# Kernel optimization log

Measured on AMD Instinct MI355X. Metric: run time of the kernel, lower is better.

The kernel has to match this reference:

```python
import jax, jax.numpy as jnp
import numpy as np

GN_EPS = 1e-5
G = 8          # SKA groups
SKS3 = 27      # sks**3


def _aff(x, s, b):
    # folded BatchNorm (eval): per-channel scale + shift on NCDHW tensor
    return x * s[None, :, None, None, None] + b[None, :, None, None, None]


def _c1(x, w):
    # 1x1x1 conv as channel GEMM; w: [O, I]
    return jnp.einsum('bcdhw,oc->bodhw', x, w)


def _dw5(x, w):
    # depthwise 5x5x5 conv, pad=2; w: [C, 1, 5, 5, 5]
    return jax.lax.conv_general_dilated(
        x, w, window_strides=(1, 1, 1), padding=[(2, 2)] * 3,
        dimension_numbers=('NCDHW', 'OIDHW', 'NCDHW'),
        feature_group_count=x.shape[1])


def setup_inputs() -> dict:
    key = jax.random.key(0)
    ks = jax.random.split(key, 24)
    B, C, D, H, W = 2, 64, 32, 32, 32

    def n(k, shape, scale=1.0):
        return jax.random.normal(k, shape, jnp.float32) * scale

    def u(k, shape):
        return jax.random.uniform(k, shape, jnp.float32, 0.5, 1.5)

    return {
        'x': n(ks[0], (B, C, D, H, W)),
        'w1': n(ks[1], (32, 64), 64 ** -0.5),
        's1': u(ks[2], (32,)), 'b1': n(ks[3], (32,), 0.1),
        'w2': n(ks[4], (32, 1, 5, 5, 5), 125 ** -0.5),
        's2': u(ks[5], (32,)), 'b2': n(ks[6], (32,), 0.1),
        'w3': n(ks[7], (32, 32), 32 ** -0.5),
        's3': u(ks[8], (32,)), 'b3': n(ks[9], (32,), 0.1),
        'w4': n(ks[10], (216, 32), 32 ** -0.5), 'b4': n(ks[11], (216,), 0.1),
        'gn_g': u(ks[12], (216,)), 'gn_b': n(ks[13], (216,), 0.1),
        'bn_s': u(ks[14], (64,)), 'bn_b': n(ks[15], (64,), 0.1),
        'pw1_w': n(ks[16], (128, 64), 64 ** -0.5),
        'pw1_s': u(ks[17], (128,)), 'pw1_b': n(ks[18], (128,), 0.1),
        'pw2_w': n(ks[19], (64, 128), 128 ** -0.5),
        'pw2_s': u(ks[20], (64,)), 'pw2_b': n(ks[21], (64,), 0.1),
    }


def reference(x, w1, s1, b1, w2, s2, b2, w3, s3, b3, w4, b4,
              gn_g, gn_b, bn_s, bn_b,
              pw1_w, pw1_s, pw1_b, pw2_w, pw2_s, pw2_b):
    B, C, D, H, W = x.shape

    # ---- LKP3D: dynamic kernel generation ----
    a = jax.nn.relu(_aff(_c1(x, w1), s1, b1))          # cv1 + BN + ReLU
    a = _aff(_dw5(a, w2), s2, b2)                      # cv2 (5^3 dw) + BN
    a = jax.nn.relu(_aff(_c1(a, w3), s3, b3))          # cv3 + BN + ReLU
    wk = _c1(a, w4) + b4[None, :, None, None, None]    # cv4: [B,216,D,H,W]
    # GroupNorm: num_groups = dim//groups = 8, channels = 216
    g = wk.reshape(B, G, SKS3, D, H, W)
    mu = g.mean(axis=(2, 3, 4, 5), keepdims=True)
    var = g.var(axis=(2, 3, 4, 5), keepdims=True)
    g = (g - mu) * jax.lax.rsqrt(var + GN_EPS)
    wk = g.reshape(B, G * SKS3, D, H, W) * gn_g[None, :, None, None, None] \
         + gn_b[None, :, None, None, None]
    wk = wk.reshape(B, G, SKS3, D, H, W)               # [B, G, 27, D, H, W]

    # ---- SKA3D: apply dynamic kernels (27 shifted copies, grouped) ----
    offs = [(di, hi, wi) for di in (-1, 0, 1) for hi in (-1, 0, 1) for wi in (-1, 0, 1)]
    patches = jnp.stack(
        [jnp.roll(x, (-di, -hi, -wi), axis=(2, 3, 4)) for di, hi, wi in offs],
        axis=2)                                        # [B, C, 27, D, H, W]
    p = patches.reshape(B, G, C // G, SKS3, D, H, W)
    sk = jnp.einsum('bgckdhw,bgkdhw->bgcdhw', p, wk).reshape(B, C, D, H, W)

    y = _aff(sk, bn_s, bn_b) + x                       # LSConv BN + residual

    # ---- FFN (residual): pw1 + BN + ReLU + pw2 + BN ----
    f = jax.nn.relu(_aff(_c1(y, pw1_w), pw1_s, pw1_b))
    f = _aff(_c1(f, pw2_w), pw2_s, pw2_b)
    return y + f
```

## Files before the change

### kernel.cpp

```cpp
#include <hip/hip_runtime.h>

#define SPAT 32768
#define BATCH 2
#define GN_EPS 1e-5f

__device__ __forceinline__ void fma4(float4& a, const float4& v, float w) {
    a.x = fmaf(v.x, w, a.x); a.y = fmaf(v.y, w, a.y);
    a.z = fmaf(v.z, w, a.z); a.w = fmaf(v.w, w, a.w);
}

__global__ __launch_bounds__(64) void k_zero(float* __restrict__ p)
{
    if (threadIdx.x < 32) p[threadIdx.x] = 0.f;
}

template <int CIN, int NO, bool RELU>
__global__ __launch_bounds__(256) void k_c1(
    const float* __restrict__ in, const float* __restrict__ w,
    const float* __restrict__ sc, const float* __restrict__ bi,
    float* __restrict__ out, int Cout)
{
    int q = blockIdx.x * 256 + threadIdx.x;
    int s = q * 4;
    int o0 = blockIdx.y * NO, b = blockIdx.z;
    const float* ip = in + (size_t)b * CIN * SPAT + s;
    float4 acc[NO];
#pragma unroll
    for (int i = 0; i < NO; ++i) acc[i] = {0.f, 0.f, 0.f, 0.f};
#pragma unroll 4
    for (int c = 0; c < CIN; ++c) {
        float4 v = *(const float4*)(ip + (size_t)c * SPAT);
#pragma unroll
        for (int i = 0; i < NO; ++i)
            fma4(acc[i], v, w[(o0 + i) * CIN + c]);
    }
#pragma unroll
    for (int i = 0; i < NO; ++i) {
        int o = o0 + i;
        float scale = sc[o], shift = bi[o];
        float4 r = acc[i];
        r.x = r.x * scale + shift; r.y = r.y * scale + shift;
        r.z = r.z * scale + shift; r.w = r.w * scale + shift;
        if (RELU) {
            r.x = fmaxf(r.x, 0.f); r.y = fmaxf(r.y, 0.f);
            r.z = fmaxf(r.z, 0.f); r.w = fmaxf(r.w, 0.f);
        }
        *(float4*)(out + ((size_t)b * Cout + o) * SPAT + s) = r;
    }
}

__global__ __launch_bounds__(256) void k_cv4_stats(
    const float* __restrict__ a, const float* __restrict__ w4,
    const float* __restrict__ b4, float* __restrict__ stats)
{
    int q = blockIdx.x * 256 + threadIdx.x;
    int s = q * 4;
    int g = blockIdx.y, b = blockIdx.z;
    const float* ip = a + (size_t)b * 32 * SPAT + s;
    const float* wg = w4 + g * 27 * 32;
    float4 wk[27];
#pragma unroll
    for (int k = 0; k < 27; ++k) {
        float bv = b4[g * 27 + k];
        wk[k] = {bv, bv, bv, bv};
    }
#pragma unroll 2
    for (int c = 0; c < 32; ++c) {
        float4 v = *(const float4*)(ip + (size_t)c * SPAT);
#pragma unroll
        for (int k = 0; k < 27; ++k)
            fma4(wk[k], v, wg[k * 32 + c]);
    }
    float sum = 0.f, ss = 0.f;
#pragma unroll
    for (int k = 0; k < 27; ++k) {
        sum += wk[k].x + wk[k].y + wk[k].z + wk[k].w;
        ss  += wk[k].x * wk[k].x + wk[k].y * wk[k].y
             + wk[k].z * wk[k].z + wk[k].w * wk[k].w;
    }
#pragma unroll
    for (int off = 32; off > 0; off >>= 1) {
        sum += __shfl_down(sum, off, 64);
        ss  += __shfl_down(ss,  off, 64);
    }
    __shared__ float sh[8];
    int wave = threadIdx.x >> 6, lane = threadIdx.x & 63;
    if (lane == 0) { sh[wave * 2] = sum; sh[wave * 2 + 1] = ss; }
    __syncthreads();
    if (threadIdx.x == 0) {
        int bg = b * 8 + g;
        atomicAdd(&stats[bg * 2 + 0], sh[0] + sh[2] + sh[4] + sh[6]);
        atomicAdd(&stats[bg * 2 + 1], sh[1] + sh[3] + sh[5] + sh[7]);
    }
}

__global__ __launch_bounds__(256) void k_ska(
    const float* __restrict__ x, const float* __restrict__ a1,
    const float* __restrict__ w4, const float* __restrict__ b4,
    const float* __restrict__ stats,
    const float* __restrict__ gn_g, const float* __restrict__ gn_b,
    const float* __restrict__ bn_s, const float* __restrict__ bn_b,
    float* __restrict__ y)
{
    int q = blockIdx.x * 256 + threadIdx.x;
    int s = q * 4;
    int g = blockIdx.y, b = blockIdx.z;
    int bg = b * 8 + g;
    const float N = 27.f * (float)SPAT;
    float mu  = stats[bg * 2 + 0] / N;
    float var = stats[bg * 2 + 1] / N - mu * mu;
    float inv = rsqrtf(var + GN_EPS);
    int d = s >> 10, h = (s >> 5) & 31, w0 = s & 31;
    int lane = threadIdx.x & 63;
    int xl_src = (lane & 56) | ((lane + 7) & 7);
    int xr_src = (lane & 56) | ((lane + 1) & 7);
    const float* xg = x + ((size_t)(b * 64 + g * 8)) * SPAT;
    const float* ag = a1 + (size_t)b * 32 * SPAT + s;
    const float* wg = w4 + g * 27 * 32;

    float4 acc[8];
    float4 xc[8];
#pragma unroll
    for (int c = 0; c < 8; ++c) acc[c] = {0.f, 0.f, 0.f, 0.f};

#pragma unroll
    for (int kd = 0; kd < 3; ++kd) {
        float4 wk9[9];
#pragma unroll
        for (int j = 0; j < 9; ++j) {
            float bv = b4[g * 27 + kd * 9 + j];
            wk9[j] = {bv, bv, bv, bv};
        }
#pragma unroll 4
        for (int c = 0; c < 32; ++c) {
            float4 v = *(const float4*)(ag + (size_t)c * SPAT);
#pragma unroll
            for (int j = 0; j < 9; ++j)
                fma4(wk9[j], v, wg[(kd * 9 + j) * 32 + c]);
        }
#pragma unroll
        for (int j = 0; j < 9; ++j) {
            int kk = kd * 9 + j;
            float gg = gn_g[g * 27 + kk] * inv;
            float sgb = gn_b[g * 27 + kk] - mu * gg;
            wk9[j].x = wk9[j].x * gg + sgb;
            wk9[j].y = wk9[j].y * gg + sgb;
            wk9[j].z = wk9[j].z * gg + sgb;
            wk9[j].w = wk9[j].w * gg + sgb;
        }
        int zd = (d + kd + 31) & 31;
#pragma unroll
        for (int kh = 0; kh < 3; ++kh) {
            int zh = (h + kh + 31) & 31;
            int rowoff = zd * 1024 + zh * 32;
            bool center = (kd == 1) && (kh == 1);
#pragma unroll
            for (int c = 0; c < 8; ++c) {
                float4 m = *(const float4*)(xg + (size_t)c * SPAT + rowoff + w0);
                if (center) xc[c] = m;
                float xl = __shfl(m.w, xl_src, 64);
                float xr = __shfl(m.x, xr_src, 64);
                float win[6] = {xl, m.x, m.y, m.z, m.w, xr};
#pragma unroll
                for (int kw = 0; kw < 3; ++kw) {
                    float4 wn = wk9[kh * 3 + kw];
                    acc[c].x = fmaf(win[0 + kw], wn.x, acc[c].x);
                    acc[c].y = fmaf(win[1 + kw], wn.y, acc[c].y);
                    acc[c].z = fmaf(win[2 + kw], wn.z, acc[c].z);
                    acc[c].w = fmaf(win[3 + kw], wn.w, acc[c].w);
                }
            }
        }
    }
#pragma unroll
    for (int c = 0; c < 8; ++c) {
        int ch = g * 8 + c;
        float bs = bn_s[ch], bb = bn_b[ch];
        float4 r;
        r.x = acc[c].x * bs + bb + xc[c].x;
        r.y = acc[c].y * bs + bb + xc[c].y;
        r.z = acc[c].z * bs + bb + xc[c].z;
        r.w = acc[c].w * bs + bb + xc[c].w;
        *(float4*)(y + ((size_t)(b * 64 + ch)) * SPAT + s) = r;
    }
}

__global__ __launch_bounds__(256) void k_dw5(
    const float* __restrict__ in, const float* __restrict__ w2,
    const float* __restrict__ s2, const float* __restrict__ b2,
    float* __restrict__ out)
{
    __shared__ float lds[8 * 36 * 40];
    int tid = threadIdx.x;
    int d0 = blockIdx.x * 4;
    int c = blockIdx.y, b = blockIdx.z;
    const float* ip = in + ((size_t)(b * 32 + c)) * SPAT;

    float4 z = {0.f, 0.f, 0.f, 0.f};
    for (int i = tid; i < 8 * 36 * 40 / 4; i += 256)
        ((float4*)lds)[i] = z;
    __syncthreads();
    for (int i = tid; i < 8 * 256; i += 256) {
        int p = i >> 8, rem = i & 255;
        int r = rem >> 3, c4 = (rem & 7) * 4;
        int d = d0 - 2 + p;
        if (d >= 0 && d < 32) {
            float4 v = *(const float4*)(ip + d * 1024 + r * 32 + c4);
            *(float4*)&lds[p * 1440 + (r + 2) * 40 + (c4 + 4)] = v;
        }
    }
    __syncthreads();

    float scl = s2[c], shf = b2[c];
    const float* wt = w2 + c * 125;
#pragma unroll
    for (int k = 0; k < 4; ++k) {
        int j = tid + k * 256;
        int pd = j >> 8, rem = j & 255;
        int hr = rem >> 3, w4i = (rem & 7) * 4;
        float4 acc = {0.f, 0.f, 0.f, 0.f};
#pragma unroll
        for (int kd = 0; kd < 5; ++kd) {
            const float* pl = &lds[(pd + kd) * 1440];
#pragma unroll
            for (int kh = 0; kh < 5; ++kh) {
                const float* row = pl + (hr + kh) * 40 + w4i;
                float4 r0 = *(const float4*)(row);
                float4 r1 = *(const float4*)(row + 4);
                float4 r2 = *(const float4*)(row + 8);
                float win[12] = {r0.x, r0.y, r0.z, r0.w,
                                 r1.x, r1.y, r1.z, r1.w,
                                 r2.x, r2.y, r2.z, r2.w};
#pragma unroll
                for (int kw = 0; kw < 5; ++kw) {
                    float wv = wt[kd * 25 + kh * 5 + kw];
                    acc.x = fmaf(wv, win[2 + 0 + kw], acc.x);
                    acc.y = fmaf(wv, win[2 + 1 + kw], acc.y);
                    acc.z = fmaf(wv, win[2 + 2 + kw], acc.z);
                    acc.w = fmaf(wv, win[2 + 3 + kw], acc.w);
                }
            }
        }
        acc.x = acc.x * scl + shf; acc.y = acc.y * scl + shf;
        acc.z = acc.z * scl + shf; acc.w = acc.w * scl + shf;
        *(float4*)(out + ((size_t)(b * 32 + c)) * SPAT
                   + (d0 + pd) * 1024 + hr * 32 + w4i) = acc;
    }
}

template <int NO>
__global__ __launch_bounds__(256) void k_pw2_out(
    const float* __restrict__ f1, const float* __restrict__ w,
    const float* __restrict__ sc, const float* __restrict__ bi,
    const float* __restrict__ yres, float* __restrict__ out)
{
    int q = blockIdx.x * 256 + threadIdx.x;
    int s = q * 4;
    int o0 = blockIdx.y * NO, b = blockIdx.z;
    const float* ip = f1 + (size_t)b * 128 * SPAT + s;
    float4 acc[NO];
#pragma unroll
    for (int i = 0; i < NO; ++i) acc[i] = {0.f, 0.f, 0.f, 0.f};
#pragma unroll 4
    for (int c = 0; c < 128; ++c) {
        float4 v = *(const float4*)(ip + (size_t)c * SPAT);
#pragma unroll
        for (int i = 0; i < NO; ++i)
            fma4(acc[i], v, w[(o0 + i) * 128 + c]);
    }
#pragma unroll
    for (int i = 0; i < NO; ++i) {
        int o = o0 + i;
        float scale = sc[o], shift = bi[o];
        float4 yv = *(const float4*)(yres + ((size_t)(b * 64 + o)) * SPAT + s);
        float4 r = acc[i];
        r.x = r.x * scale + shift + yv.x;
        r.y = r.y * scale + shift + yv.y;
        r.z = r.z * scale + shift + yv.z;
        r.w = r.w * scale + shift + yv.w;
        *(float4*)(out + ((size_t)(b * 64 + o)) * SPAT + s) = r;
    }
}

extern "C" void kernel_launch(void* const* d_in, const int* in_sizes, int n_in,
                              void* d_out, int out_size, void* d_ws, size_t ws_size,
                              hipStream_t stream)
{
    const float* x     = (const float*)d_in[0];
    const float* w1    = (const float*)d_in[1];
    const float* s1    = (const float*)d_in[2];
    const float* b1    = (const float*)d_in[3];
    const float* w2    = (const float*)d_in[4];
    const float* s2    = (const float*)d_in[5];
    const float* b2    = (const float*)d_in[6];
    const float* w3    = (const float*)d_in[7];
    const float* s3    = (const float*)d_in[8];
    const float* b3    = (const float*)d_in[9];
    const float* w4    = (const float*)d_in[10];
    const float* b4    = (const float*)d_in[11];
    const float* gn_g  = (const float*)d_in[12];
    const float* gn_b  = (const float*)d_in[13];
    const float* bn_s  = (const float*)d_in[14];
    const float* bn_b  = (const float*)d_in[15];
    const float* pw1_w = (const float*)d_in[16];
    const float* pw1_s = (const float*)d_in[17];
    const float* pw1_b = (const float*)d_in[18];
    const float* pw2_w = (const float*)d_in[19];
    const float* pw2_s = (const float*)d_in[20];
    const float* pw2_b = (const float*)d_in[21];

    float* ws    = (float*)d_ws;
    float* a1    = ws;
    float* a2    = a1 + (size_t)BATCH * 32 * SPAT;
    float* yb    = a2 + (size_t)BATCH * 32 * SPAT;
    float* f1    = yb + (size_t)BATCH * 64 * SPAT;
    float* stats = f1 + (size_t)BATCH * 128 * SPAT;

    dim3 blk(256);
    k_zero<<<dim3(1), dim3(64), 0, stream>>>(stats);
    k_c1<64, 8, true><<<dim3(SPAT / 1024, 4, BATCH), blk, 0, stream>>>(
        x, w1, s1, b1, a1, 32);
    k_dw5<<<dim3(8, 32, BATCH), blk, 0, stream>>>(a1, w2, s2, b2, a2);
    k_c1<32, 8, true><<<dim3(SPAT / 1024, 4, BATCH), blk, 0, stream>>>(
        a2, w3, s3, b3, a1, 32);
    k_cv4_stats<<<dim3(SPAT / 1024, 8, BATCH), blk, 0, stream>>>(
        a1, w4, b4, stats);
    k_ska<<<dim3(SPAT / 1024, 8, BATCH), blk, 0, stream>>>(
        x, a1, w4, b4, stats, gn_g, gn_b, bn_s, bn_b, yb);
    k_c1<64, 16, true><<<dim3(SPAT / 1024, 8, BATCH), blk, 0, stream>>>(
        yb, pw1_w, pw1_s, pw1_b, f1, 128);
    k_pw2_out<16><<<dim3(SPAT / 1024, 4, BATCH), blk, 0, stream>>>(
        f1, pw2_w, pw2_s, pw2_b, yb, (float*)d_out);
}
```

Before: 266.2 us.

## Compute GroupNorm stats via Gram matrix and halve per-thread work across kernels

The GroupNorm statistics are no longer computed by materialising all 216 cv4 outputs per voxel. Instead a Gram matrix and channel sums of the 32-channel activation are accumulated per block, and a single-block kernel derives the mean and variance algebraically from w4 and b4. It also switches all pointwise and SKA kernels from float4 to float2 per thread with more blocks and occupancy hints, and halves the dw5 depth tile. Risks are an extra serial single-block reduction kernel, fp32 cancellation in the E[x²]-mu² variance, and more launches and thinner threads.

```diff
diff --git a/kernel.cpp b/kernel.cpp
--- a/kernel.cpp
+++ b/kernel.cpp
@@ -4,97 +4,128 @@
 #define BATCH 2
 #define GN_EPS 1e-5f
 
-__device__ __forceinline__ void fma4(float4& a, const float4& v, float w) {
+__device__ __forceinline__ void fma2(float2& a, const float2& v, float w) {
     a.x = fmaf(v.x, w, a.x); a.y = fmaf(v.y, w, a.y);
-    a.z = fmaf(v.z, w, a.z); a.w = fmaf(v.w, w, a.w);
-}
-
-__global__ __launch_bounds__(64) void k_zero(float* __restrict__ p)
-{
-    if (threadIdx.x < 32) p[threadIdx.x] = 0.f;
-}
-
-template <int CIN, int NO, bool RELU>
-__global__ __launch_bounds__(256) void k_c1(
+}
+
+template <int CIN, int NO, bool RELU, int MINW>
+__global__ __launch_bounds__(256, MINW) void k_c1(
     const float* __restrict__ in, const float* __restrict__ w,
     const float* __restrict__ sc, const float* __restrict__ bi,
     float* __restrict__ out, int Cout)
 {
     int q = blockIdx.x * 256 + threadIdx.x;
-    int s = q * 4;
     int o0 = blockIdx.y * NO, b = blockIdx.z;
-    const float* ip = in + (size_t)b * CIN * SPAT + s;
-    float4 acc[NO];
-#pragma unroll
-    for (int i = 0; i < NO; ++i) acc[i] = {0.f, 0.f, 0.f, 0.f};
+    const float2* ip = (const float2*)(in + (size_t)b * CIN * SPAT) + q;
+    float2 acc[NO];
+#pragma unroll
+    for (int i = 0; i < NO; ++i) acc[i] = {0.f, 0.f};
 #pragma unroll 4
     for (int c = 0; c < CIN; ++c) {
-        float4 v = *(const float4*)(ip + (size_t)c * SPAT);
+        float2 v = ip[(size_t)c * (SPAT / 2)];
 #pragma unroll
         for (int i = 0; i < NO; ++i)
-            fma4(acc[i], v, w[(o0 + i) * CIN + c]);
-    }
+            fma2(acc[i], v, w[(o0 + i) * CIN + c]);
+    }
+    float2* op = (float2*)(out + (size_t)b * Cout * SPAT) + q;
 #pragma unroll
     for (int i = 0; i < NO; ++i) {
         int o = o0 + i;
         float scale = sc[o], shift = bi[o];
-        float4 r = acc[i];
+        float2 r = acc[i];
         r.x = r.x * scale + shift; r.y = r.y * scale + shift;
-        r.z = r.z * scale + shift; r.w = r.w * scale + shift;
-        if (RELU) {
-            r.x = fmaxf(r.x, 0.f); r.y = fmaxf(r.y, 0.f);
-            r.z = fmaxf(r.z, 0.f); r.w = fmaxf(r.w, 0.f);
-        }
-        *(float4*)(out + ((size_t)b * Cout + o) * SPAT + s) = r;
-    }
-}
-
-__global__ __launch_bounds__(256) void k_cv4_stats(
-    const float* __restrict__ a, const float* __restrict__ w4,
+        if (RELU) { r.x = fmaxf(r.x, 0.f); r.y = fmaxf(r.y, 0.f); }
+        op[(size_t)o * (SPAT / 2)] = r;
+    }
+}
+
+__global__ __launch_bounds__(256) void k_gram(
+    const float* __restrict__ a, float* __restrict__ partial)
+{
+    __shared__ float lds[32 * 257];
+    int blk = blockIdx.x, b = blockIdx.z;
+    const float* ap = a + (size_t)b * 32 * SPAT + blk * 256;
+    for (int i = threadIdx.x; i < 32 * 64; i += 256) {
+        int m = i >> 6, p4 = (i & 63) * 4;
+        float4 v = *(const float4*)(ap + (size_t)m * SPAT + p4);
+        lds[m * 257 + p4 + 0] = v.x; lds[m * 257 + p4 + 1] = v.y;
+        lds[m * 257 + p4 + 2] = v.z; lds[m * 257 + p4 + 3] = v.w;
+    }
+    __syncthreads();
+    float* outp = partial + (size_t)(b * 128 + blk) * 1056;
+#pragma unroll
+    for (int it = 0; it < 4; ++it) {
+        int pid = threadIdx.x + it * 256;
+        const float* pa = &lds[(pid >> 5) * 257];
+        const float* pb = &lds[(pid & 31) * 257];
+        float acc = 0.f;
+#pragma unroll 8
+        for (int p = 0; p < 256; ++p) acc = fmaf(pa[p], pb[p], acc);
+        outp[pid] = acc;
+    }
+    if (threadIdx.x < 32) {
+        const float* pa = &lds[threadIdx.x * 257];
+        float scc = 0.f;
+#pragma unroll 8
+        for (int p = 0; p < 256; ++p) scc += pa[p];
+        outp[1024 + threadIdx.x] = scc;
+    }
+}
+
+__global__ __launch_bounds__(512) void k_stats(
+    const float* __restrict__ partial, const float* __restrict__ w4,
     const float* __restrict__ b4, float* __restrict__ stats)
 {
-    int q = blockIdx.x * 256 + threadIdx.x;
-    int s = q * 4;
-    int g = blockIdx.y, b = blockIdx.z;
-    const float* ip = a + (size_t)b * 32 * SPAT + s;
-    const float* wg = w4 + g * 27 * 32;
-    float4 wk[27];
-#pragma unroll
-    for (int k = 0; k < 27; ++k) {
-        float bv = b4[g * 27 + k];
-        wk[k] = {bv, bv, bv, bv};
-    }
-#pragma unroll 2
-    for (int c = 0; c < 32; ++c) {
-        float4 v = *(const float4*)(ip + (size_t)c * SPAT);
-#pragma unroll
-        for (int k = 0; k < 27; ++k)
-            fma4(wk[k], v, wg[k * 32 + c]);
-    }
-    float sum = 0.f, ss = 0.f;
-#pragma unroll
-    for (int k = 0; k < 27; ++k) {
-        sum += wk[k].x + wk[k].y + wk[k].z + wk[k].w;
-        ss  += wk[k].x * wk[k].x + wk[k].y * wk[k].y
-             + wk[k].z * wk[k].z + wk[k].w * wk[k].w;
-    }
-#pragma unroll
-    for (int off = 32; off > 0; off >>= 1) {
-        sum += __shfl_down(sum, off, 64);
-        ss  += __shfl_down(ss,  off, 64);
-    }
-    __shared__ float sh[8];
-    int wave = threadIdx.x >> 6, lane = threadIdx.x & 63;
-    if (lane == 0) { sh[wave * 2] = sum; sh[wave * 2 + 1] = ss; }
-    __syncthreads();
-    if (threadIdx.x == 0) {
-        int bg = b * 8 + g;
-        atomicAdd(&stats[bg * 2 + 0], sh[0] + sh[2] + sh[4] + sh[6]);
-        atomicAdd(&stats[bg * 2 + 1], sh[1] + sh[3] + sh[5] + sh[7]);
-    }
-}
-
-__global__ __launch_bounds__(256) void k_ska(
+    __shared__ float G[2 * 1056];
+    __shared__ float sred[432], ssred[432];
+    for (int e = threadIdx.x; e < 2 * 1056; e += 512) {
+        int b = e / 1056, pid = e % 1056;
+        float acc = 0.f;
+#pragma unroll 8
+        for (int blk = 0; blk < 128; ++blk)
+            acc += partial[(size_t)(b * 128 + blk) * 1056 + pid];
+        G[e] = acc;
+    }
+    __syncthreads();
+    if (threadIdx.x < 432) {
+        int t = threadIdx.x;
+        int b = t / 216, r = t % 216, g = r / 27, k = r % 27;
+        const float* wk = w4 + (g * 27 + k) * 32;
+        float wreg[32];
+#pragma unroll
+        for (int m = 0; m < 32; ++m) wreg[m] = wk[m];
+        const float* Gb = &G[b * 1056];
+        const float* Sb = &G[b * 1056 + 1024];
+        float sk = 0.f, ssk = 0.f;
+#pragma unroll
+        for (int m = 0; m < 32; ++m) {
+            sk = fmaf(wreg[m], Sb[m], sk);
+            float dot = 0.f;
+#pragma unroll
+            for (int mm = 0; mm < 32; ++mm)
+                dot = fmaf(wreg[mm], Gb[m * 32 + mm], dot);
+            ssk = fmaf(wreg[m], dot, ssk);
+        }
+        float bb = b4[g * 27 + k];
+        float NN = (float)SPAT;
+        ssk += 2.f * bb * sk + NN * bb * bb;
+        sk  += NN * bb;
+        sred[t] = sk; ssred[t] = ssk;
+    }
+    __syncthreads();
+    if (threadIdx.x < 16) {
+        int bg = threadIdx.x;
+        float s = 0.f, ss = 0.f;
+        for (int k = 0; k < 27; ++k) { s += sred[bg * 27 + k]; ss += ssred[bg * 27 + k]; }
+        float N27 = 27.f * (float)SPAT;
+        float mu = s / N27;
+        float var = ss / N27 - mu * mu;
+        stats[bg * 2 + 0] = mu;
+        stats[bg * 2 + 1] = rsqrtf(var + GN_EPS);
+    }
+}
+
+__global__ __launch_bounds__(256, 4) void k_ska(
     const float* __restrict__ x, const float* __restrict__ a1,
     const float* __restrict__ w4, const float* __restrict__ b4,
     const float* __restrict__ stats,
@@ -103,104 +134,102 @@
     float* __restrict__ y)
 {
     int q = blockIdx.x * 256 + threadIdx.x;
-    int s = q * 4;
+    int s2 = q * 2;
     int g = blockIdx.y, b = blockIdx.z;
     int bg = b * 8 + g;
-    const float N = 27.f * (float)SPAT;
-    float mu  = stats[bg * 2 + 0] / N;
-    float var = stats[bg * 2 + 1] / N - mu * mu;
-    float inv = rsqrtf(var + GN_EPS);
-    int d = s >> 10, h = (s >> 5) & 31, w0 = s & 31;
+    float mu  = stats[bg * 2 + 0];
+    float inv = stats[bg * 2 + 1];
+    int d = s2 >> 10, h = (s2 >> 5) & 31, w0 = s2 & 31;
     int lane = threadIdx.x & 63;
-    int xl_src = (lane & 56) | ((lane + 7) & 7);
-    int xr_src = (lane & 56) | ((lane + 1) & 7);
-    const float* xg = x + ((size_t)(b * 64 + g * 8)) * SPAT;
-    const float* ag = a1 + (size_t)b * 32 * SPAT + s;
+    int xl_src = (lane & 48) | ((lane + 15) & 15);
+    int xr_src = (lane & 48) | ((lane + 1) & 15);
+    const float2* xg = (const float2*)(x + (size_t)(b * 64 + g * 8) * SPAT);
+    const float2* ag = (const float2*)(a1 + (size_t)b * 32 * SPAT) + q;
     const float* wg = w4 + g * 27 * 32;
 
-    float4 acc[8];
-    float4 xc[8];
-#pragma unroll
-    for (int c = 0; c < 8; ++c) acc[c] = {0.f, 0.f, 0.f, 0.f};
+    float2 acc[8];
+#pragma unroll
+    for (int c = 0; c < 8; ++c) acc[c] = {0.f, 0.f};
 
 #pragma unroll
     for (int kd = 0; kd < 3; ++kd) {
-        float4 wk9[9];
+        float2 wk9[9];
 #pragma unroll
         for (int j = 0; j < 9; ++j) {
             float bv = b4[g * 27 + kd * 9 + j];
-            wk9[j] = {bv, bv, bv, bv};
-        }
-#pragma unroll 4
+            wk9[j] = {bv, bv};
+        }
+#pragma unroll 8
         for (int c = 0; c < 32; ++c) {
-            float4 v = *(const float4*)(ag + (size_t)c * SPAT);
+            float2 v = ag[(size_t)c * (SPAT / 2)];
 #pragma unroll
             for (int j = 0; j < 9; ++j)
-                fma4(wk9[j], v, wg[(kd * 9 + j) * 32 + c]);
+                fma2(wk9[j], v, wg[(kd * 9 + j) * 32 + c]);
         }
 #pragma unroll
         for (int j = 0; j < 9; ++j) {
             int kk = kd * 9 + j;
-            float gg = gn_g[g * 27 + kk] * inv;
-            float sgb = gn_b[g * 27 + kk] - mu * gg;
-            wk9[j].x = wk9[j].x * gg + sgb;
-            wk9[j].y = wk9[j].y * gg + sgb;
-            wk9[j].z = wk9[j].z * gg + sgb;
-            wk9[j].w = wk9[j].w * gg + sgb;
+            float A = gn_g[g * 27 + kk] * inv;
+            float B = gn_b[g * 27 + kk] - mu * A;
+            wk9[j].x = wk9[j].x * A + B;
+            wk9[j].y = wk9[j].y * A + B;
         }
         int zd = (d + kd + 31) & 31;
 #pragma unroll
         for (int kh = 0; kh < 3; ++kh) {
             int zh = (h + kh + 31) & 31;
-            int rowoff = zd * 1024 + zh * 32;
-            bool center = (kd == 1) && (kh == 1);
+            int ro2 = (zd * 1024 + zh * 32 + w0) >> 1;
+            float2 m[8];
+#pragma unroll
+            for (int c = 0; c < 8; ++c)
+                m[c] = xg[(size_t)c * (SPAT / 2) + ro2];
+            float xl[8], xr[8];
 #pragma unroll
             for (int c = 0; c < 8; ++c) {
-                float4 m = *(const float4*)(xg + (size_t)c * SPAT + rowoff + w0);
-                if (center) xc[c] = m;
-                float xl = __shfl(m.w, xl_src, 64);
-                float xr = __shfl(m.x, xr_src, 64);
-                float win[6] = {xl, m.x, m.y, m.z, m.w, xr};
+                xl[c] = __shfl(m[c].y, xl_src, 64);
+                xr[c] = __shfl(m[c].x, xr_src, 64);
+            }
+#pragma unroll
+            for (int c = 0; c < 8; ++c) {
+                float win[4] = {xl[c], m[c].x, m[c].y, xr[c]};
 #pragma unroll
                 for (int kw = 0; kw < 3; ++kw) {
-                    float4 wn = wk9[kh * 3 + kw];
-                    acc[c].x = fmaf(win[0 + kw], wn.x, acc[c].x);
-                    acc[c].y = fmaf(win[1 + kw], wn.y, acc[c].y);
-                    acc[c].z = fmaf(win[2 + kw], wn.z, acc[c].z);
-                    acc[c].w = fmaf(win[3 + kw], wn.w, acc[c].w);
+                    float2 wn = wk9[kh * 3 + kw];
+                    acc[c].x = fmaf(win[kw],     wn.x, acc[c].x);
+                    acc[c].y = fmaf(win[kw + 1], wn.y, acc[c].y);
                 }
             }
         }
     }
+    float2* yp = (float2*)(y + (size_t)(b * 64 + g * 8) * SPAT) + q - (size_t)0;
 #pragma unroll
     for (int c = 0; c < 8; ++c) {
         int ch = g * 8 + c;
         float bs = bn_s[ch], bb = bn_b[ch];
-        float4 r;
-        r.x = acc[c].x * bs + bb + xc[c].x;
-        r.y = acc[c].y * bs + bb + xc[c].y;
-        r.z = acc[c].z * bs + bb + xc[c].z;
-        r.w = acc[c].w * bs + bb + xc[c].w;
-        *(float4*)(y + ((size_t)(b * 64 + ch)) * SPAT + s) = r;
-    }
-}
-
-__global__ __launch_bounds__(256) void k_dw5(
+        float2 xc = xg[(size_t)c * (SPAT / 2) + q];
+        float2 r;
+        r.x = acc[c].x * bs + bb + xc.x;
+        r.y = acc[c].y * bs + bb + xc.y;
+        *((float2*)((float*)yp + (size_t)c * SPAT)) = r;
+    }
+}
+
+__global__ __launch_bounds__(256, 4) void k_dw5(
     const float* __restrict__ in, const float* __restrict__ w2,
     const float* __restrict__ s2, const float* __restrict__ b2,
     float* __restrict__ out)
 {
-    __shared__ float lds[8 * 36 * 40];
+    __shared__ float lds[6 * 36 * 40];
     int tid = threadIdx.x;
-    int d0 = blockIdx.x * 4;
+    int d0 = blockIdx.x * 2;
     int c = blockIdx.y, b = blockIdx.z;
     const float* ip = in + ((size_t)(b * 32 + c)) * SPAT;
 
     float4 z = {0.f, 0.f, 0.f, 0.f};
-    for (int i = tid; i < 8 * 36 * 40 / 4; i += 256)
+    for (int i = tid; i < 6 * 36 * 40 / 4; i += 256)
         ((float4*)lds)[i] = z;
     __syncthreads();
-    for (int i = tid; i < 8 * 256; i += 256) {
+    for (int i = tid; i < 6 * 256; i += 256) {
         int p = i >> 8, rem = i & 255;
         int r = rem >> 3, c4 = (rem & 7) * 4;
         int d = d0 - 2 + p;
@@ -214,7 +243,7 @@
     float scl = s2[c], shf = b2[c];
     const float* wt = w2 + c * 125;
 #pragma unroll
-    for (int k = 0; k < 4; ++k) {
+    for (int k = 0; k < 2; ++k) {
         int j = tid + k * 256;
         int pd = j >> 8, rem = j & 255;
         int hr = rem >> 3, w4i = (rem & 7) * 4;
@@ -249,36 +278,35 @@
 }
 
 template <int NO>
-__global__ __launch_bounds__(256) void k_pw2_out(
+__global__ __launch_bounds__(256, 4) void k_pw2_out(
     const float* __restrict__ f1, const float* __restrict__ w,
     const float* __restrict__ sc, const float* __restrict__ bi,
     const float* __restrict__ yres, float* __restrict__ out)
 {
     int q = blockIdx.x * 256 + threadIdx.x;
-    int s = q * 4;
     int o0 = blockIdx.y * NO, b = blockIdx.z;
-    const float* ip = f1 + (size_t)b * 128 * SPAT + s;
-    float4 acc[NO];
-#pragma unroll
-    for (int i = 0; i < NO; ++i) acc[i] = {0.f, 0.f, 0.f, 0.f};
+    const float2* ip = (const float2*)(f1 + (size_t)b * 128 * SPAT) + q;
+    float2 acc[NO];
+#pragma unroll
+    for (int i = 0; i < NO; ++i) acc[i] = {0.f, 0.f};
 #pragma unroll 4
     for (int c = 0; c < 128; ++c) {
-        float4 v = *(const float4*)(ip + (size_t)c * SPAT);
+        float2 v = ip[(size_t)c * (SPAT / 2)];
 #pragma unroll
         for (int i = 0; i < NO; ++i)
-            fma4(acc[i], v, w[(o0 + i) * 128 + c]);
-    }
+            fma2(acc[i], v, w[(o0 + i) * 128 + c]);
+    }
+    const float2* yp = (const float2*)(yres + (size_t)b * 64 * SPAT) + q;
+    float2* op = (float2*)(out + (size_t)b * 64 * SPAT) + q;
 #pragma unroll
     for (int i = 0; i < NO; ++i) {
         int o = o0 + i;
         float scale = sc[o], shift = bi[o];
-        float4 yv = *(const float4*)(yres + ((size_t)(b * 64 + o)) * SPAT + s);
-        float4 r = acc[i];
+        float2 yv = yp[(size_t)o * (SPAT / 2)];
+        float2 r = acc[i];
         r.x = r.x * scale + shift + yv.x;
         r.y = r.y * scale + shift + yv.y;
-        r.z = r.z * scale + shift + yv.z;
-        r.w = r.w * scale + shift + yv.w;
-        *(float4*)(out + ((size_t)(b * 64 + o)) * SPAT + s) = r;
+        op[(size_t)o * (SPAT / 2)] = r;
     }
 }
 
@@ -314,21 +342,21 @@
     float* a2    = a1 + (size_t)BATCH * 32 * SPAT;
     float* yb    = a2 + (size_t)BATCH * 32 * SPAT;
     float* f1    = yb + (size_t)BATCH * 64 * SPAT;
-    float* stats = f1 + (size_t)BATCH * 128 * SPAT;
+    float* part  = f1 + (size_t)BATCH * 128 * SPAT;
+    float* stats = part + (size_t)256 * 1056;
 
     dim3 blk(256);
-    k_zero<<<dim3(1), dim3(64), 0, stream>>>(stats);
-    k_c1<64, 8, true><<<dim3(SPAT / 1024, 4, BATCH), blk, 0, stream>>>(
+    k_c1<64, 4, true, 4><<<dim3(SPAT / 512, 8, BATCH), blk, 0, stream>>>(
         x, w1, s1, b1, a1, 32);
-    k_dw5<<<dim3(8, 32, BATCH), blk, 0, stream>>>(a1, w2, s2, b2, a2);
-    k_c1<32, 8, true><<<dim3(SPAT / 1024, 4, BATCH), blk, 0, stream>>>(
+    k_dw5<<<dim3(16, 32, BATCH), blk, 0, stream>>>(a1, w2, s2, b2, a2);
+    k_c1<32, 4, true, 4><<<dim3(SPAT / 512, 8, BATCH), blk, 0, stream>>>(
         a2, w3, s3, b3, a1, 32);
-    k_cv4_stats<<<dim3(SPAT / 1024, 8, BATCH), blk, 0, stream>>>(
-        a1, w4, b4, stats);
-    k_ska<<<dim3(SPAT / 1024, 8, BATCH), blk, 0, stream>>>(
+    k_gram<<<dim3(128, 1, BATCH), blk, 0, stream>>>(a1, part);
+    k_stats<<<dim3(1), dim3(512), 0, stream>>>(part, w4, b4, stats);
+    k_ska<<<dim3(SPAT / 512, 8, BATCH), blk, 0, stream>>>(
         x, a1, w4, b4, stats, gn_g, gn_b, bn_s, bn_b, yb);
-    k_c1<64, 16, true><<<dim3(SPAT / 1024, 8, BATCH), blk, 0, stream>>>(
+    k_c1<64, 8, true, 6><<<dim3(SPAT / 512, 16, BATCH), blk, 0, stream>>>(
         yb, pw1_w, pw1_s, pw1_b, f1, 128);
-    k_pw2_out<16><<<dim3(SPAT / 1024, 4, BATCH), blk, 0, stream>>>(
+    k_pw2_out<8><<<dim3(SPAT / 512, 8, BATCH), blk, 0, stream>>>(
         f1, pw2_w, pw2_s, pw2_b, yb, (float*)d_out);
 }
```

New measurement: 362.8 us. +36.3%, slower.
